# Performance work log

Hardware: AMD Instinct MI355X
Metric: run time of the kernel (lower is better)

Reference implementation:

```python
import jax, jax.numpy as jnp
import numpy as np

N_RAYS = 262144
HIDDEN = 256
NEAR, FAR, MAX_ITERS, EPS = 1.0, 10.0, 64, 1e-5


def setup_inputs() -> dict:
    key = jax.random.key(0)
    k1, k2, k3, k4 = jax.random.split(key, 4)
    # camera at z=-4 looking toward +z; sphere of radius 1.5 at origin
    origins = jnp.array([0.0, 0.0, -4.0]) + 0.01 * jax.random.normal(k1, (N_RAYS, 3), jnp.float32)
    d = jnp.array([0.0, 0.0, 1.0]) + 0.15 * jax.random.normal(k2, (N_RAYS, 3), jnp.float32)
    directions = d / jnp.linalg.norm(d, axis=-1, keepdims=True)
    center = jnp.zeros((3,), jnp.float32)
    radius = jnp.full((1,), 1.5, jnp.float32)
    w1 = jax.random.normal(k3, (3, HIDDEN), jnp.float32) * (1.0 / np.sqrt(3.0))
    b1 = jnp.zeros((HIDDEN,), jnp.float32)
    w2 = jax.random.normal(k4, (HIDDEN, 3), jnp.float32) * (1.0 / np.sqrt(HIDDEN))
    b2 = jnp.zeros((3,), jnp.float32)
    return {"origins": origins, "directions": directions, "center": center,
            "radius": radius, "w1": w1, "b1": b1, "w2": w2, "b2": b2}


def reference(origins, directions, center, radius, w1, b1, w2, b2):
    def sdf(p):  # [N,3] -> [N,1]
        return jnp.linalg.norm(p - center, axis=-1, keepdims=True) - radius

    t0 = jnp.full_like(origins[:, :1], NEAR)          # [N,1]
    p0 = origins + t0 * directions                     # [N,3]
    m0 = jnp.ones_like(t0, dtype=bool)                 # [N,1]

    def step(state, _):
        t, pts, mask, cont = state
        f_p = sdf(pts)
        t_new = t + f_p
        pts_new = origins + t_new * directions
        mask_new = mask & (t_new <= FAR)               # mask[t>far] = False (sticky)
        new_cont = cont & jnp.any((f_p > EPS) & mask_new)
        # apply this iteration's update only if the torch while-loop was still running
        t = jnp.where(cont, t_new, t)
        pts = jnp.where(cont, pts_new, pts)
        mask = jnp.where(cont, mask_new, mask)
        return (t, pts, mask, new_cont), None

    (t, pts, mask, _), _ = jax.lax.scan(step, (t0, p0, m0, jnp.array(True)), None, length=MAX_ITERS)

    # color: MLP on intersection points, zeroed for rays that never hit
    h = jax.nn.relu(pts @ w1 + b1)
    rgb = jax.nn.sigmoid(h @ w2 + b2)                  # [N,3]
    color = jnp.where(mask, rgb, 0.0)
    return color
```

## Files before the change

kernel.cpp:

```cpp
#include <hip/hip_runtime.h>
#include <math.h>

#define N_RAYS   262144
#define HIDDEN   256
#define NEAR_T   1.0f
#define FAR_T    10.0f
#define MAX_IT   64
#define EPS_T    1e-5f

__global__ __launch_bounds__(256)
void st_fused(const float* __restrict__ org,
              const float* __restrict__ dir,
              const float* __restrict__ center,
              const float* __restrict__ radius,
              const float* __restrict__ w1,
              const float* __restrict__ b1,
              const float* __restrict__ w2,
              const float* __restrict__ b2,
              float* __restrict__ out) {
    const int r = blockIdx.x * blockDim.x + threadIdx.x;

    const float cx = center[0], cy = center[1], cz = center[2];
    const float rad = radius[0];

    const float ox = org[3*r+0], oy = org[3*r+1], oz = org[3*r+2];
    const float dx = dir[3*r+0], dy = dir[3*r+1], dz = dir[3*r+2];

    const float qx = ox - cx, qy = oy - cy, qz = oz - cz;
    const float B  = qx*dx + qy*dy + qz*dz;
    const float ex = __builtin_fmaf(-B, dx, qx);
    const float ey = __builtin_fmaf(-B, dy, qy);
    const float ez = __builtin_fmaf(-B, dz, qz);
    const float C  = ex*ex + ey*ey + ez*ez;

    float u = NEAR_T + B;
    #pragma unroll
    for (int i = 0; i < MAX_IT; ++i) {
        const float f = __builtin_amdgcn_sqrtf(__builtin_fmaf(u, u, C)) - rad;
        u += f;
    }
    const float t   = u - B;
    const bool  hit = (t <= FAR_T);

    const float px = __builtin_fmaf(t, dx, ox);
    const float py = __builtin_fmaf(t, dy, oy);
    const float pz = __builtin_fmaf(t, dz, oz);

    float a0 = b2[0], a1 = b2[1], a2 = b2[2];
    #pragma unroll 16
    for (int j = 0; j < HIDDEN; ++j) {
        float h = __builtin_fmaf(px, w1[0*HIDDEN + j],
                  __builtin_fmaf(py, w1[1*HIDDEN + j],
                  __builtin_fmaf(pz, w1[2*HIDDEN + j], b1[j])));
        h = fmaxf(h, 0.0f);
        a0 = __builtin_fmaf(h, w2[3*j+0], a0);
        a1 = __builtin_fmaf(h, w2[3*j+1], a1);
        a2 = __builtin_fmaf(h, w2[3*j+2], a2);
    }

    const float s0 = 1.0f / (1.0f + __expf(-a0));
    const float s1 = 1.0f / (1.0f + __expf(-a1));
    const float s2 = 1.0f / (1.0f + __expf(-a2));

    out[3*r+0] = hit ? s0 : 0.0f;
    out[3*r+1] = hit ? s1 : 0.0f;
    out[3*r+2] = hit ? s2 : 0.0f;
}

extern "C" void kernel_launch(void* const* d_in, const int* in_sizes, int n_in,
                              void* d_out, int out_size, void* d_ws, size_t ws_size,
                              hipStream_t stream) {
    const float* org    = (const float*)d_in[0];
    const float* dir    = (const float*)d_in[1];
    const float* center = (const float*)d_in[2];
    const float* radius = (const float*)d_in[3];
    const float* w1     = (const float*)d_in[4];
    const float* b1     = (const float*)d_in[5];
    const float* w2     = (const float*)d_in[6];
    const float* b2     = (const float*)d_in[7];
    float* out = (float*)d_out;

    const int block = 256;
    const int grid  = N_RAYS / block;

    st_fused<<<grid, block, 0, stream>>>(org, dir, center, radius,
                                         w1, b1, w2, b2, out);
}
```

Baseline: 88.88 us.

## Stage MLP weights in shared memory and process two rays per thread

Packs w1/b1 and w2 into float4 records in LDS at block start, then has each thread trace and shade two rays (one from each half of the ray array). Each weight load is reused for two rays and the two independent sqrt iteration chains can interleave for more ILP. The cost is higher register pressure, an extra sync, and half as many blocks, which reduces available parallelism; the LDS reads may also be slower than the uniform scalar loads the compiler could use before.

```diff
diff --git a/kernel.cpp b/kernel.cpp
--- a/kernel.cpp
+++ b/kernel.cpp
@@ -6,65 +6,111 @@
 #define NEAR_T   1.0f
 #define FAR_T    10.0f
 #define MAX_IT   64
-#define EPS_T    1e-5f
 
-__global__ __launch_bounds__(256)
-void st_fused(const float* __restrict__ org,
-              const float* __restrict__ dir,
-              const float* __restrict__ center,
-              const float* __restrict__ radius,
-              const float* __restrict__ w1,
-              const float* __restrict__ b1,
-              const float* __restrict__ w2,
-              const float* __restrict__ b2,
-              float* __restrict__ out) {
-    const int r = blockIdx.x * blockDim.x + threadIdx.x;
+#define RPT    2
+#define BLOCK  256
+#define HALF   (N_RAYS / 2)
+
+__global__ __launch_bounds__(BLOCK)
+void st_fused2(const float* __restrict__ org,
+               const float* __restrict__ dir,
+               const float* __restrict__ center,
+               const float* __restrict__ radius,
+               const float* __restrict__ w1,
+               const float* __restrict__ b1,
+               const float* __restrict__ w2,
+               const float* __restrict__ b2,
+               float* __restrict__ out) {
+    __shared__ float4 s_rec[2 * HIDDEN];
+
+    for (int j = threadIdx.x; j < HIDDEN; j += BLOCK) {
+        s_rec[2*j+0] = make_float4(w1[j], w1[HIDDEN + j], w1[2*HIDDEN + j], b1[j]);
+        s_rec[2*j+1] = make_float4(w2[3*j+0], w2[3*j+1], w2[3*j+2], 0.0f);
+    }
+    __syncthreads();
+
+    const int rA = blockIdx.x * BLOCK + threadIdx.x;
+    const int rB = rA + HALF;
 
     const float cx = center[0], cy = center[1], cz = center[2];
     const float rad = radius[0];
 
-    const float ox = org[3*r+0], oy = org[3*r+1], oz = org[3*r+2];
-    const float dx = dir[3*r+0], dy = dir[3*r+1], dz = dir[3*r+2];
+    const float oxA = org[3*rA+0], oyA = org[3*rA+1], ozA = org[3*rA+2];
+    const float dxA = dir[3*rA+0], dyA = dir[3*rA+1], dzA = dir[3*rA+2];
+    const float oxB = org[3*rB+0], oyB = org[3*rB+1], ozB = org[3*rB+2];
+    const float dxB = dir[3*rB+0], dyB = dir[3*rB+1], dzB = dir[3*rB+2];
 
-    const float qx = ox - cx, qy = oy - cy, qz = oz - cz;
-    const float B  = qx*dx + qy*dy + qz*dz;
-    const float ex = __builtin_fmaf(-B, dx, qx);
-    const float ey = __builtin_fmaf(-B, dy, qy);
-    const float ez = __builtin_fmaf(-B, dz, qz);
-    const float C  = ex*ex + ey*ey + ez*ez;
+    const float qxA = oxA - cx, qyA = oyA - cy, qzA = ozA - cz;
+    const float BA  = qxA*dxA + qyA*dyA + qzA*dzA;
+    const float exA = __builtin_fmaf(-BA, dxA, qxA);
+    const float eyA = __builtin_fmaf(-BA, dyA, qyA);
+    const float ezA = __builtin_fmaf(-BA, dzA, qzA);
+    const float CA  = exA*exA + eyA*eyA + ezA*ezA;
 
-    float u = NEAR_T + B;
+    const float qxB = oxB - cx, qyB = oyB - cy, qzB = ozB - cz;
+    const float BB  = qxB*dxB + qyB*dyB + qzB*dzB;
+    const float exB = __builtin_fmaf(-BB, dxB, qxB);
+    const float eyB = __builtin_fmaf(-BB, dyB, qyB);
+    const float ezB = __builtin_fmaf(-BB, dzB, qzB);
+    const float CB  = exB*exB + eyB*eyB + ezB*ezB;
+
+    float uA = NEAR_T + BA;
+    float uB = NEAR_T + BB;
     #pragma unroll
     for (int i = 0; i < MAX_IT; ++i) {
-        const float f = __builtin_amdgcn_sqrtf(__builtin_fmaf(u, u, C)) - rad;
-        u += f;
+        const float fA = __builtin_amdgcn_sqrtf(__builtin_fmaf(uA, uA, CA)) - rad;
+        const float fB = __builtin_amdgcn_sqrtf(__builtin_fmaf(uB, uB, CB)) - rad;
+        uA += fA;
+        uB += fB;
     }
-    const float t   = u - B;
-    const bool  hit = (t <= FAR_T);
+    const float tA = uA - BA, tB = uB - BB;
+    const bool hitA = (tA <= FAR_T), hitB = (tB <= FAR_T);
 
-    const float px = __builtin_fmaf(t, dx, ox);
-    const float py = __builtin_fmaf(t, dy, oy);
-    const float pz = __builtin_fmaf(t, dz, oz);
+    const float pxA = __builtin_fmaf(tA, dxA, oxA);
+    const float pyA = __builtin_fmaf(tA, dyA, oyA);
+    const float pzA = __builtin_fmaf(tA, dzA, ozA);
+    const float pxB = __builtin_fmaf(tB, dxB, oxB);
+    const float pyB = __builtin_fmaf(tB, dyB, oyB);
+    const float pzB = __builtin_fmaf(tB, dzB, ozB);
 
-    float a0 = b2[0], a1 = b2[1], a2 = b2[2];
+    const float bb0 = b2[0], bb1 = b2[1], bb2 = b2[2];
+    float a0A = bb0, a1A = bb1, a2A = bb2;
+    float a0B = bb0, a1B = bb1, a2B = bb2;
+
+    const float4* __restrict__ rec = s_rec;
     #pragma unroll 16
     for (int j = 0; j < HIDDEN; ++j) {
-        float h = __builtin_fmaf(px, w1[0*HIDDEN + j],
-                  __builtin_fmaf(py, w1[1*HIDDEN + j],
-                  __builtin_fmaf(pz, w1[2*HIDDEN + j], b1[j])));
-        h = fmaxf(h, 0.0f);
-        a0 = __builtin_fmaf(h, w2[3*j+0], a0);
-        a1 = __builtin_fmaf(h, w2[3*j+1], a1);
-        a2 = __builtin_fmaf(h, w2[3*j+2], a2);
+        const float4 lo = rec[2*j+0];
+        const float4 hi = rec[2*j+1];
+        float hA = __builtin_fmaf(pxA, lo.x,
+                   __builtin_fmaf(pyA, lo.y,
+                   __builtin_fmaf(pzA, lo.z, lo.w)));
+        float hB = __builtin_fmaf(pxB, lo.x,
+                   __builtin_fmaf(pyB, lo.y,
+                   __builtin_fmaf(pzB, lo.z, lo.w)));
+        hA = fmaxf(hA, 0.0f);
+        hB = fmaxf(hB, 0.0f);
+        a0A = __builtin_fmaf(hA, hi.x, a0A);
+        a1A = __builtin_fmaf(hA, hi.y, a1A);
+        a2A = __builtin_fmaf(hA, hi.z, a2A);
+        a0B = __builtin_fmaf(hB, hi.x, a0B);
+        a1B = __builtin_fmaf(hB, hi.y, a1B);
+        a2B = __builtin_fmaf(hB, hi.z, a2B);
     }
 
-    const float s0 = 1.0f / (1.0f + __expf(-a0));
-    const float s1 = 1.0f / (1.0f + __expf(-a1));
-    const float s2 = 1.0f / (1.0f + __expf(-a2));
+    const float s0A = 1.0f / (1.0f + __expf(-a0A));
+    const float s1A = 1.0f / (1.0f + __expf(-a1A));
+    const float s2A = 1.0f / (1.0f + __expf(-a2A));
+    const float s0B = 1.0f / (1.0f + __expf(-a0B));
+    const float s1B = 1.0f / (1.0f + __expf(-a1B));
+    const float s2B = 1.0f / (1.0f + __expf(-a2B));
 
-    out[3*r+0] = hit ? s0 : 0.0f;
-    out[3*r+1] = hit ? s1 : 0.0f;
-    out[3*r+2] = hit ? s2 : 0.0f;
+    out[3*rA+0] = hitA ? s0A : 0.0f;
+    out[3*rA+1] = hitA ? s1A : 0.0f;
+    out[3*rA+2] = hitA ? s2A : 0.0f;
+    out[3*rB+0] = hitB ? s0B : 0.0f;
+    out[3*rB+1] = hitB ? s1B : 0.0f;
+    out[3*rB+2] = hitB ? s2B : 0.0f;
 }
 
 extern "C" void kernel_launch(void* const* d_in, const int* in_sizes, int n_in,
@@ -80,9 +126,7 @@
     const float* b2     = (const float*)d_in[7];
     float* out = (float*)d_out;
 
-    const int block = 256;
-    const int grid  = N_RAYS / block;
-
-    st_fused<<<grid, block, 0, stream>>>(org, dir, center, radius,
-                                         w1, b1, w2, b2, out);
+    const int grid = HALF / BLOCK;
+    st_fused2<<<grid, BLOCK, 0, stream>>>(org, dir, center, radius,
+                                          w1, b1, w2, b2, out);
 }
```

Measured after the change: 91.33 us. 2.7% more time.

## Process four rays per thread with weights staged in shared memory

Applied to the files above, without the earlier changes.

Each thread now marches and shades four rays strided across the batch, interleaving their independent sqrt iteration chains and reusing each MLP weight load across four rays. The MLP weights are staged into LDS as float4 vectors once per block. This aims to raise instruction-level parallelism and cut weight-fetch overhead, at the cost of more registers and a grid four times smaller, which lowers wave occupancy.

```diff
diff --git a/kernel.cpp b/kernel.cpp
--- a/kernel.cpp
+++ b/kernel.cpp
@@ -6,65 +6,134 @@
 #define NEAR_T   1.0f
 #define FAR_T    10.0f
 #define MAX_IT   64
-#define EPS_T    1e-5f
 
-__global__ __launch_bounds__(256)
-void st_fused(const float* __restrict__ org,
-              const float* __restrict__ dir,
-              const float* __restrict__ center,
-              const float* __restrict__ radius,
-              const float* __restrict__ w1,
-              const float* __restrict__ b1,
-              const float* __restrict__ w2,
-              const float* __restrict__ b2,
-              float* __restrict__ out) {
-    const int r = blockIdx.x * blockDim.x + threadIdx.x;
+#define RPT     4
+#define BLOCK   256
+#define STRIDE  (N_RAYS / RPT)
+#define JQ      (HIDDEN / 4)
+
+__global__ __launch_bounds__(BLOCK)
+void st_fused4(const float* __restrict__ org,
+               const float* __restrict__ dir,
+               const float* __restrict__ center,
+               const float* __restrict__ radius,
+               const float* __restrict__ w1,
+               const float* __restrict__ b1,
+               const float* __restrict__ w2,
+               const float* __restrict__ b2,
+               float* __restrict__ out) {
+    __shared__ float4 s_wx[JQ], s_wy[JQ], s_wz[JQ], s_wb[JQ];
+    __shared__ float4 s_wa[JQ], s_wv[JQ], s_wc[JQ];
+
+    {
+        const int j = threadIdx.x;
+        ((float*)s_wx)[j] = w1[0*HIDDEN + j];
+        ((float*)s_wy)[j] = w1[1*HIDDEN + j];
+        ((float*)s_wz)[j] = w1[2*HIDDEN + j];
+        ((float*)s_wb)[j] = b1[j];
+        ((float*)s_wa)[j] = w2[3*j+0];
+        ((float*)s_wv)[j] = w2[3*j+1];
+        ((float*)s_wc)[j] = w2[3*j+2];
+    }
+    __syncthreads();
+
+    const int r0 = blockIdx.x * BLOCK + threadIdx.x;
 
     const float cx = center[0], cy = center[1], cz = center[2];
     const float rad = radius[0];
 
-    const float ox = org[3*r+0], oy = org[3*r+1], oz = org[3*r+2];
-    const float dx = dir[3*r+0], dy = dir[3*r+1], dz = dir[3*r+2];
+    float px[RPT], py[RPT], pz[RPT];
+    bool  hit[RPT];
 
-    const float qx = ox - cx, qy = oy - cy, qz = oz - cz;
-    const float B  = qx*dx + qy*dy + qz*dz;
-    const float ex = __builtin_fmaf(-B, dx, qx);
-    const float ey = __builtin_fmaf(-B, dy, qy);
-    const float ez = __builtin_fmaf(-B, dz, qz);
-    const float C  = ex*ex + ey*ey + ez*ez;
-
-    float u = NEAR_T + B;
-    #pragma unroll
-    for (int i = 0; i < MAX_IT; ++i) {
-        const float f = __builtin_amdgcn_sqrtf(__builtin_fmaf(u, u, C)) - rad;
-        u += f;
-    }
-    const float t   = u - B;
-    const bool  hit = (t <= FAR_T);
-
-    const float px = __builtin_fmaf(t, dx, ox);
-    const float py = __builtin_fmaf(t, dy, oy);
-    const float pz = __builtin_fmaf(t, dz, oz);
-
-    float a0 = b2[0], a1 = b2[1], a2 = b2[2];
-    #pragma unroll 16
-    for (int j = 0; j < HIDDEN; ++j) {
-        float h = __builtin_fmaf(px, w1[0*HIDDEN + j],
-                  __builtin_fmaf(py, w1[1*HIDDEN + j],
-                  __builtin_fmaf(pz, w1[2*HIDDEN + j], b1[j])));
-        h = fmaxf(h, 0.0f);
-        a0 = __builtin_fmaf(h, w2[3*j+0], a0);
-        a1 = __builtin_fmaf(h, w2[3*j+1], a1);
-        a2 = __builtin_fmaf(h, w2[3*j+2], a2);
+    {
+        float Bq[RPT], Cq[RPT], u[RPT];
+        float dxs[RPT], dys[RPT], dzs[RPT], oxs[RPT], oys[RPT], ozs[RPT];
+        #pragma unroll
+        for (int k = 0; k < RPT; ++k) {
+            const int r = r0 + k * STRIDE;
+            const float ox = org[3*r+0], oy = org[3*r+1], oz = org[3*r+2];
+            const float dx = dir[3*r+0], dy = dir[3*r+1], dz = dir[3*r+2];
+            oxs[k]=ox; oys[k]=oy; ozs[k]=oz; dxs[k]=dx; dys[k]=dy; dzs[k]=dz;
+            const float qx = ox - cx, qy = oy - cy, qz = oz - cz;
+            const float B  = qx*dx + qy*dy + qz*dz;
+            const float ex = __builtin_fmaf(-B, dx, qx);
+            const float ey = __builtin_fmaf(-B, dy, qy);
+            const float ez = __builtin_fmaf(-B, dz, qz);
+            Bq[k] = B;
+            Cq[k] = ex*ex + ey*ey + ez*ez;
+            u[k]  = NEAR_T + B;
+        }
+        #pragma unroll
+        for (int i = 0; i < MAX_IT; ++i) {
+            #pragma unroll
+            for (int k = 0; k < RPT; ++k) {
+                const float f = __builtin_amdgcn_sqrtf(
+                                    __builtin_fmaf(u[k], u[k], Cq[k])) - rad;
+                u[k] += f;
+            }
+        }
+        #pragma unroll
+        for (int k = 0; k < RPT; ++k) {
+            const float t = u[k] - Bq[k];
+            hit[k] = (t <= FAR_T);
+            px[k] = __builtin_fmaf(t, dxs[k], oxs[k]);
+            py[k] = __builtin_fmaf(t, dys[k], oys[k]);
+            pz[k] = __builtin_fmaf(t, dzs[k], ozs[k]);
+        }
     }
 
-    const float s0 = 1.0f / (1.0f + __expf(-a0));
-    const float s1 = 1.0f / (1.0f + __expf(-a1));
-    const float s2 = 1.0f / (1.0f + __expf(-a2));
+    const float bb0 = b2[0], bb1 = b2[1], bb2 = b2[2];
+    float a0[RPT], a1[RPT], a2[RPT];
+    #pragma unroll
+    for (int k = 0; k < RPT; ++k) { a0[k]=bb0; a1[k]=bb1; a2[k]=bb2; }
 
-    out[3*r+0] = hit ? s0 : 0.0f;
-    out[3*r+1] = hit ? s1 : 0.0f;
-    out[3*r+2] = hit ? s2 : 0.0f;
+    #pragma unroll 2
+    for (int jq = 0; jq < JQ; ++jq) {
+        const float4 wx = s_wx[jq], wy = s_wy[jq], wz = s_wz[jq], wb = s_wb[jq];
+        const float4 wa = s_wa[jq], wv = s_wv[jq], wc = s_wc[jq];
+        #pragma unroll
+        for (int k = 0; k < RPT; ++k) {
+            float h;
+            h = __builtin_fmaf(px[k], wx.x, __builtin_fmaf(py[k], wy.x,
+                __builtin_fmaf(pz[k], wz.x, wb.x)));
+            h = fmaxf(h, 0.0f);
+            a0[k] = __builtin_fmaf(h, wa.x, a0[k]);
+            a1[k] = __builtin_fmaf(h, wv.x, a1[k]);
+            a2[k] = __builtin_fmaf(h, wc.x, a2[k]);
+
+            h = __builtin_fmaf(px[k], wx.y, __builtin_fmaf(py[k], wy.y,
+                __builtin_fmaf(pz[k], wz.y, wb.y)));
+            h = fmaxf(h, 0.0f);
+            a0[k] = __builtin_fmaf(h, wa.y, a0[k]);
+            a1[k] = __builtin_fmaf(h, wv.y, a1[k]);
+            a2[k] = __builtin_fmaf(h, wc.y, a2[k]);
+
+            h = __builtin_fmaf(px[k], wx.z, __builtin_fmaf(py[k], wy.z,
+                __builtin_fmaf(pz[k], wz.z, wb.z)));
+            h = fmaxf(h, 0.0f);
+            a0[k] = __builtin_fmaf(h, wa.z, a0[k]);
+            a1[k] = __builtin_fmaf(h, wv.z, a1[k]);
+            a2[k] = __builtin_fmaf(h, wc.z, a2[k]);
+
+            h = __builtin_fmaf(px[k], wx.w, __builtin_fmaf(py[k], wy.w,
+                __builtin_fmaf(pz[k], wz.w, wb.w)));
+            h = fmaxf(h, 0.0f);
+            a0[k] = __builtin_fmaf(h, wa.w, a0[k]);
+            a1[k] = __builtin_fmaf(h, wv.w, a1[k]);
+            a2[k] = __builtin_fmaf(h, wc.w, a2[k]);
+        }
+    }
+
+    #pragma unroll
+    for (int k = 0; k < RPT; ++k) {
+        const int r = r0 + k * STRIDE;
+        const float s0 = 1.0f / (1.0f + __expf(-a0[k]));
+        const float s1 = 1.0f / (1.0f + __expf(-a1[k]));
+        const float s2 = 1.0f / (1.0f + __expf(-a2[k]));
+        out[3*r+0] = hit[k] ? s0 : 0.0f;
+        out[3*r+1] = hit[k] ? s1 : 0.0f;
+        out[3*r+2] = hit[k] ? s2 : 0.0f;
+    }
 }
 
 extern "C" void kernel_launch(void* const* d_in, const int* in_sizes, int n_in,
@@ -80,9 +149,7 @@
     const float* b2     = (const float*)d_in[7];
     float* out = (float*)d_out;
 
-    const int block = 256;
-    const int grid  = N_RAYS / block;
-
-    st_fused<<<grid, block, 0, stream>>>(org, dir, center, radius,
-                                         w1, b1, w2, b2, out);
+    const int grid = N_RAYS / (BLOCK * RPT);
+    st_fused4<<<grid, BLOCK, 0, stream>>>(org, dir, center, radius,
+                                          w1, b1, w2, b2, out);
 }
```

Result: no change. 88.86 us (-0.0%).

## Split ray trace and MLP into two kernels with LDS-staged weights

Applied to the files above, without the earlier changes.

Splits the fused kernel in two. The first kernel runs the sphere-trace and writes each ray's hit point and hit flag as a float4 to workspace. The second kernel stages the MLP weights in shared memory as float4 vectors, processes 4 rays per thread so each weight load is reused, and software-prefetches the next weight group. The aim is to cut the per-ray global/scalar weight loads in the MLP loop, at the cost of an extra launch and a round trip through workspace memory.

```diff
diff --git a/kernel.cpp b/kernel.cpp
--- a/kernel.cpp
+++ b/kernel.cpp
@@ -6,18 +6,13 @@
 #define NEAR_T   1.0f
 #define FAR_T    10.0f
 #define MAX_IT   64
-#define EPS_T    1e-5f
 
 __global__ __launch_bounds__(256)
-void st_fused(const float* __restrict__ org,
+void st_trace(const float* __restrict__ org,
               const float* __restrict__ dir,
               const float* __restrict__ center,
               const float* __restrict__ radius,
-              const float* __restrict__ w1,
-              const float* __restrict__ b1,
-              const float* __restrict__ w2,
-              const float* __restrict__ b2,
-              float* __restrict__ out) {
+              float4* __restrict__ ws_p) {
     const int r = blockIdx.x * blockDim.x + threadIdx.x;
 
     const float cx = center[0], cy = center[1], cz = center[2];
@@ -40,31 +35,109 @@
         u += f;
     }
     const float t   = u - B;
-    const bool  hit = (t <= FAR_T);
+    const float hit = (t <= FAR_T) ? 1.0f : 0.0f;
 
-    const float px = __builtin_fmaf(t, dx, ox);
-    const float py = __builtin_fmaf(t, dy, oy);
-    const float pz = __builtin_fmaf(t, dz, oz);
+    ws_p[r] = make_float4(__builtin_fmaf(t, dx, ox),
+                          __builtin_fmaf(t, dy, oy),
+                          __builtin_fmaf(t, dz, oz),
+                          hit);
+}
 
-    float a0 = b2[0], a1 = b2[1], a2 = b2[2];
-    #pragma unroll 16
-    for (int j = 0; j < HIDDEN; ++j) {
-        float h = __builtin_fmaf(px, w1[0*HIDDEN + j],
-                  __builtin_fmaf(py, w1[1*HIDDEN + j],
-                  __builtin_fmaf(pz, w1[2*HIDDEN + j], b1[j])));
-        h = fmaxf(h, 0.0f);
-        a0 = __builtin_fmaf(h, w2[3*j+0], a0);
-        a1 = __builtin_fmaf(h, w2[3*j+1], a1);
-        a2 = __builtin_fmaf(h, w2[3*j+2], a2);
+#define RPT   4
+#define JQ    (HIDDEN / 4)
+
+__global__ __launch_bounds__(256)
+void st_mlp(const float4* __restrict__ ws_p,
+            const float* __restrict__ w1,
+            const float* __restrict__ b1,
+            const float* __restrict__ w2,
+            const float* __restrict__ b2,
+            float* __restrict__ out) {
+    __shared__ float4 s_wx[JQ], s_wy[JQ], s_wz[JQ], s_wb[JQ];
+    __shared__ float4 s_wa[JQ], s_wv[JQ], s_wc[JQ];
+
+    {
+        const int j = threadIdx.x;
+        ((float*)s_wx)[j] = w1[0*HIDDEN + j];
+        ((float*)s_wy)[j] = w1[1*HIDDEN + j];
+        ((float*)s_wz)[j] = w1[2*HIDDEN + j];
+        ((float*)s_wb)[j] = b1[j];
+        ((float*)s_wa)[j] = w2[3*j+0];
+        ((float*)s_wv)[j] = w2[3*j+1];
+        ((float*)s_wc)[j] = w2[3*j+2];
+    }
+    __syncthreads();
+
+    const int base = blockIdx.x * (256 * RPT) + threadIdx.x;
+
+    float px[RPT], py[RPT], pz[RPT], hf[RPT];
+    #pragma unroll
+    for (int k = 0; k < RPT; ++k) {
+        const float4 p = ws_p[base + k * 256];
+        px[k] = p.x; py[k] = p.y; pz[k] = p.z; hf[k] = p.w;
     }
 
-    const float s0 = 1.0f / (1.0f + __expf(-a0));
-    const float s1 = 1.0f / (1.0f + __expf(-a1));
-    const float s2 = 1.0f / (1.0f + __expf(-a2));
+    const float bb0 = b2[0], bb1 = b2[1], bb2 = b2[2];
+    float a0[RPT], a1[RPT], a2[RPT];
+    #pragma unroll
+    for (int k = 0; k < RPT; ++k) { a0[k]=bb0; a1[k]=bb1; a2[k]=bb2; }
 
-    out[3*r+0] = hit ? s0 : 0.0f;
-    out[3*r+1] = hit ? s1 : 0.0f;
-    out[3*r+2] = hit ? s2 : 0.0f;
+    float4 cwx = s_wx[0], cwy = s_wy[0], cwz = s_wz[0], cwb = s_wb[0];
+    float4 cwa = s_wa[0], cwv = s_wv[0], cwc = s_wc[0];
+
+    #pragma unroll 4
+    for (int jq = 0; jq < JQ; ++jq) {
+        float4 nwx, nwy, nwz, nwb, nwa, nwv, nwc;
+        if (jq + 1 < JQ) {
+            nwx = s_wx[jq+1]; nwy = s_wy[jq+1]; nwz = s_wz[jq+1]; nwb = s_wb[jq+1];
+            nwa = s_wa[jq+1]; nwv = s_wv[jq+1]; nwc = s_wc[jq+1];
+        }
+        #pragma unroll
+        for (int k = 0; k < RPT; ++k) {
+            float h;
+            h = __builtin_fmaf(px[k], cwx.x, __builtin_fmaf(py[k], cwy.x,
+                __builtin_fmaf(pz[k], cwz.x, cwb.x)));
+            h = fmaxf(h, 0.0f);
+            a0[k] = __builtin_fmaf(h, cwa.x, a0[k]);
+            a1[k] = __builtin_fmaf(h, cwv.x, a1[k]);
+            a2[k] = __builtin_fmaf(h, cwc.x, a2[k]);
+
+            h = __builtin_fmaf(px[k], cwx.y, __builtin_fmaf(py[k], cwy.y,
+                __builtin_fmaf(pz[k], cwz.y, cwb.y)));
+            h = fmaxf(h, 0.0f);
+            a0[k] = __builtin_fmaf(h, cwa.y, a0[k]);
+            a1[k] = __builtin_fmaf(h, cwv.y, a1[k]);
+            a2[k] = __builtin_fmaf(h, cwc.y, a2[k]);
+
+            h = __builtin_fmaf(px[k], cwx.z, __builtin_fmaf(py[k], cwy.z,
+                __builtin_fmaf(pz[k], cwz.z, cwb.z)));
+            h = fmaxf(h, 0.0f);
+            a0[k] = __builtin_fmaf(h, cwa.z, a0[k]);
+            a1[k] = __builtin_fmaf(h, cwv.z, a1[k]);
+            a2[k] = __builtin_fmaf(h, cwc.z, a2[k]);
+
+            h = __builtin_fmaf(px[k], cwx.w, __builtin_fmaf(py[k], cwy.w,
+                __builtin_fmaf(pz[k], cwz.w, cwb.w)));
+            h = fmaxf(h, 0.0f);
+            a0[k] = __builtin_fmaf(h, cwa.w, a0[k]);
+            a1[k] = __builtin_fmaf(h, cwv.w, a1[k]);
+            a2[k] = __builtin_fmaf(h, cwc.w, a2[k]);
+        }
+        cwx = nwx; cwy = nwy; cwz = nwz; cwb = nwb;
+        cwa = nwa; cwv = nwv; cwc = nwc;
+    }
+
+    #pragma unroll
+    for (int k = 0; k < RPT; ++k) {
+        const int r = base + k * 256;
+        const bool hit = (hf[k] != 0.0f);
+        const float s0 = 1.0f / (1.0f + __expf(-a0[k]));
+        const float s1 = 1.0f / (1.0f + __expf(-a1[k]));
+        const float s2 = 1.0f / (1.0f + __expf(-a2[k]));
+        out[3*r+0] = hit ? s0 : 0.0f;
+        out[3*r+1] = hit ? s1 : 0.0f;
+        out[3*r+2] = hit ? s2 : 0.0f;
+    }
 }
 
 extern "C" void kernel_launch(void* const* d_in, const int* in_sizes, int n_in,
@@ -80,9 +153,8 @@
     const float* b2     = (const float*)d_in[7];
     float* out = (float*)d_out;
 
-    const int block = 256;
-    const int grid  = N_RAYS / block;
+    float4* ws_p = (float4*)d_ws;
 
-    st_fused<<<grid, block, 0, stream>>>(org, dir, center, radius,
-                                         w1, b1, w2, b2, out);
+    st_trace<<<N_RAYS / 256, 256, 0, stream>>>(org, dir, center, radius, ws_p);
+    st_mlp<<<N_RAYS / (256 * RPT), 256, 0, stream>>>(ws_p, w1, b1, w2, b2, out);
 }
```

Result: slower. 91.51 us (+3.0%).
